# Performance work log

Measured on AMD Instinct MI355X. Metric: run time of the kernel, lower is better.

The kernel has to match this reference:

```python
import jax, jax.numpy as jnp
import numpy as np

B, CIN, H, W = 8, 4, 512, 512
HID, NCLS = 32, 19
WIN = 3
SCALE = 2


def conv(x, w, b, stride):
    # torch Conv2d(kernel=3, padding=1, stride=stride) equivalent
    y = jax.lax.conv_general_dilated(
        x, w, (stride, stride), [(1, 1), (1, 1)],
        dimension_numbers=('NCHW', 'OIHW', 'NCHW'))
    return y + b[None, :, None, None]


def interp_matrix(n_in, n_out, dtype):
    # 1D bilinear interpolation matrix, align_corners=True semantics
    pos = jnp.arange(n_out, dtype=dtype) * ((n_in - 1) / (n_out - 1))
    lo = jnp.clip(jnp.floor(pos).astype(jnp.int32), 0, n_in - 2)
    frac = pos - lo.astype(dtype)
    M = jnp.zeros((n_out, n_in), dtype)
    M = M.at[jnp.arange(n_out), lo].add(1 - frac)
    M = M.at[jnp.arange(n_out), lo + 1].add(frac)
    return M


def setup_inputs() -> dict:
    key = jax.random.key(0)
    ks = jax.random.split(key, 3)
    x = jax.random.normal(ks[0], (B, CIN, H, W), jnp.float32)
    w1 = jax.random.normal(ks[1], (HID, CIN, 3, 3), jnp.float32) * 0.1
    b1 = jnp.zeros((HID,), jnp.float32)
    w2 = jax.random.normal(ks[2], (NCLS, HID, 3, 3), jnp.float32) * 0.1
    b2 = jnp.zeros((NCLS,), jnp.float32)
    return {"x": x, "w1": w1, "b1": b1, "w2": w2, "b2": b2}


def reference(x, w1, b1, w2, b2):
    # --- cnn backbone -> class response maps ---
    h = jax.nn.relu(conv(x, w1, b1, 2))          # [B, HID, H/2, W/2]
    cmaps = conv(h, w2, b2, 1)                   # [B, NCLS, H/2, W/2]

    # --- bilinear upsample, align_corners=True (scale_factor=2) ---
    hi, wi = cmaps.shape[2], cmaps.shape[3]
    Mh = interp_matrix(hi, hi * SCALE, cmaps.dtype)
    Mw = interp_matrix(wi, wi * SCALE, cmaps.dtype)
    cmaps = jnp.einsum('oh,bchw,pw->bcop', Mh, cmaps, Mw)  # [B, NCLS, H, W]

    # --- peak stimulation: 3x3 local-max with -inf padding ---
    neg_inf = jnp.asarray(-jnp.inf, cmaps.dtype)
    local_max = jax.lax.reduce_window(
        cmaps, neg_inf, jax.lax.max,
        (1, 1, WIN, WIN), (1, 1, 1, 1),
        [(0, 0), (0, 0), (1, 1), (1, 1)])

    # median filter: per-(batch, class) spatial median threshold
    med = jnp.median(cmaps.reshape(cmaps.shape[0], cmaps.shape[1], -1), axis=2)
    med = med[:, :, None, None]

    peak_map = (cmaps == local_max) & (cmaps >= med)       # bool peak mask
    pf = peak_map.astype(cmaps.dtype)

    # aggregation: mean of map values at peaks -> class logits [B, NCLS]
    logits = (cmaps * pf).sum(axis=(2, 3)) / pf.sum(axis=(2, 3))
    return cmaps, logits
```

## Files before the change

kernel.cpp:

```cpp
#include <hip/hip_runtime.h>

#define B_ 8
#define CIN_ 4
#define H_ 512
#define W_ 512
#define HID_ 32
#define NCLS_ 19
#define HO_ 256
#define WO_ 256
#define UP_ 512
#define NPLANE (B_*NCLS_)
#define PLANE_ELEMS (UP_*UP_)
#define KMED1 131071u


__device__ __forceinline__ unsigned f2key(float f) {
  unsigned u = __float_as_uint(f);
  return (u & 0x80000000u) ? ~u : (u | 0x80000000u);
}
__device__ __forceinline__ float key2f(unsigned k) {
  unsigned u = (k & 0x80000000u) ? (k & 0x7FFFFFFFu) : ~k;
  return __uint_as_float(u);
}
__device__ __forceinline__ float ninf() { return __uint_as_float(0xFF800000u); }

__device__ __forceinline__ float up_val(const float* __restrict__ p, int oy, int ox) {
  const float s = (float)(255.0 / 511.0);
  float posy = (float)oy * s;
  int ly = (int)posy; if (ly > 254) ly = 254;
  float fy = posy - (float)ly;
  float posx = (float)ox * s;
  int lx = (int)posx; if (lx > 254) lx = 254;
  float fx = posx - (float)lx;
  const float* q = p + ly * WO_ + lx;
  float a = q[0], b = q[1], c = q[WO_], d = q[WO_ + 1];
  float r0 = fmaf(fx, b - a, a);
  float r1 = fmaf(fx, d - c, c);
  return fmaf(fy, r1 - r0, r0);
}

__global__ __launch_bounds__(256, 4) void conv1_kernel(
    const float* __restrict__ x, const float* __restrict__ w1,
    const float* __restrict__ b1, float* __restrict__ h) {
  int t = threadIdx.x & 63;
  int r = threadIdx.x >> 6;
  int oh = blockIdx.x * 4 + r;
  int b  = blockIdx.z;
  int ow0 = blockIdx.y * 128 + t * 2;
  int ic0 = 2 * ow0;

  float2 acc[HID_];
  #pragma unroll
  for (int oc = 0; oc < HID_; ++oc) {
    float bb = b1[oc];
    acc[oc].x = bb; acc[oc].y = bb;
  }

  #pragma unroll
  for (int ci = 0; ci < CIN_; ++ci) {
    const float* xp = x + ((size_t)(b * CIN_ + ci)) * H_ * W_;
    float4 A0, A1, A2;
    float lm[3];
    #pragma unroll
    for (int kh = 0; kh < 3; ++kh) {
      int ih = 2 * oh + kh - 1;
      float4 Av; float lv = 0.f;
      if ((unsigned)ih < (unsigned)H_) {
        const float* row = xp + ih * W_;
        Av = *reinterpret_cast<const float4*>(row + ic0);
        lv = (ic0 > 0) ? row[ic0 - 1] : 0.f;
      } else {
        Av.x = 0.f; Av.y = 0.f; Av.z = 0.f; Av.w = 0.f;
      }
      if (kh == 0) A0 = Av; else if (kh == 1) A1 = Av; else A2 = Av;
      lm[kh] = lv;
    }
    #pragma unroll
    for (int oc = 0; oc < HID_; ++oc) {
      const float* wp = w1 + ((size_t)oc * CIN_ + ci) * 9;
      {
        float w0 = wp[0], w1v = wp[1], w2v = wp[2];
        acc[oc].x += w0 * lm[0] + w1v * A0.x + w2v * A0.y;
        acc[oc].y += w0 * A0.y  + w1v * A0.z + w2v * A0.w;
      }
      {
        float w0 = wp[3], w1v = wp[4], w2v = wp[5];
        acc[oc].x += w0 * lm[1] + w1v * A1.x + w2v * A1.y;
        acc[oc].y += w0 * A1.y  + w1v * A1.z + w2v * A1.w;
      }
      {
        float w0 = wp[6], w1v = wp[7], w2v = wp[8];
        acc[oc].x += w0 * lm[2] + w1v * A2.x + w2v * A2.y;
        acc[oc].y += w0 * A2.y  + w1v * A2.z + w2v * A2.w;
      }
    }
  }
  #pragma unroll
  for (int oc = 0; oc < HID_; ++oc) {
    float2 o;
    o.x = fmaxf(acc[oc].x, 0.f); o.y = fmaxf(acc[oc].y, 0.f);
    *reinterpret_cast<float2*>(h + (((size_t)(b * HID_ + oc) * HO_ + oh) * WO_ + ow0)) = o;
  }
}

__global__ __launch_bounds__(256, 4) void conv2_kernel(
    const float* __restrict__ h, const float* __restrict__ w2,
    const float* __restrict__ b2, float* __restrict__ c0) {
  int t = threadIdx.x & 63;
  int r = threadIdx.x >> 6;
  int oh = blockIdx.x * 4 + r;
  int b  = blockIdx.z;
  int ow0 = blockIdx.y * 128 + t * 2;

  float2 acc[NCLS_];
  #pragma unroll
  for (int oc = 0; oc < NCLS_; ++oc) {
    float bb = b2[oc];
    acc[oc].x = bb; acc[oc].y = bb;
  }

  for (int ci = 0; ci < HID_; ++ci) {
    const float* hp = h + ((size_t)(b * HID_ + ci)) * HO_ * WO_;
    float2 M0, M1, M2;
    float L[3], R[3];
    #pragma unroll
    for (int kh = 0; kh < 3; ++kh) {
      int ih = oh + kh - 1;
      float2 Mv;
      float lv = 0.f, rv = 0.f;
      if ((unsigned)ih < (unsigned)HO_) {
        const float* row = hp + ih * WO_;
        Mv = *reinterpret_cast<const float2*>(row + ow0);
        lv = (ow0 > 0) ? row[ow0 - 1] : 0.f;
        rv = (ow0 + 2 < WO_) ? row[ow0 + 2] : 0.f;
      } else {
        Mv.x = 0.f; Mv.y = 0.f;
      }
      if (kh == 0) M0 = Mv; else if (kh == 1) M1 = Mv; else M2 = Mv;
      L[kh] = lv; R[kh] = rv;
    }
    const float* wpc = w2 + ci * 9;
    #pragma unroll
    for (int oc = 0; oc < NCLS_; ++oc) {
      const float* wp = wpc + oc * (HID_ * 9);
      {
        float w0 = wp[0], w1v = wp[1], w2v = wp[2];
        acc[oc].x += w0 * L[0]  + w1v * M0.x + w2v * M0.y;
        acc[oc].y += w0 * M0.x + w1v * M0.y + w2v * R[0];
      }
      {
        float w0 = wp[3], w1v = wp[4], w2v = wp[5];
        acc[oc].x += w0 * L[1]  + w1v * M1.x + w2v * M1.y;
        acc[oc].y += w0 * M1.x + w1v * M1.y + w2v * R[1];
      }
      {
        float w0 = wp[6], w1v = wp[7], w2v = wp[8];
        acc[oc].x += w0 * L[2]  + w1v * M2.x + w2v * M2.y;
        acc[oc].y += w0 * M2.x + w1v * M2.y + w2v * R[2];
      }
    }
  }
  #pragma unroll
  for (int oc = 0; oc < NCLS_; ++oc) {
    *reinterpret_cast<float2*>(c0 + (((size_t)(b * NCLS_ + oc) * HO_ + oh) * WO_ + ow0)) = acc[oc];
  }
}

__global__ __launch_bounds__(256) void upsample_kernel(
    const float* __restrict__ c0, float* __restrict__ out) {
  int tid = threadIdx.x;
  int oy = blockIdx.x * 2 + (tid >> 7);
  int t = tid & 127;
  int plane = blockIdx.y;
  const float* p = c0 + (size_t)plane * HO_ * WO_;
  int ox0 = t * 4;
  float4 o;
  o.x = up_val(p, oy, ox0 + 0);
  o.y = up_val(p, oy, ox0 + 1);
  o.z = up_val(p, oy, ox0 + 2);
  o.w = up_val(p, oy, ox0 + 3);
  *reinterpret_cast<float4*>(out + ((size_t)plane * UP_ + oy) * UP_ + ox0) = o;
}


__global__ void init_kernel(unsigned* kArr, unsigned* pvalArr, unsigned* gbArr,
                            unsigned* flagArr) {
  int i = threadIdx.x;
  if (i < NPLANE) { kArr[i] = KMED1; pvalArr[i] = 0u; gbArr[i] = 0u; flagArr[i] = 0u; }
}

__global__ __launch_bounds__(256) void hist_pass_kernel(
    const float* __restrict__ up, const unsigned* __restrict__ pvalArr,
    unsigned* __restrict__ ghist, int shift, unsigned bmask, unsigned fmask) {
  __shared__ unsigned lh[4 * 2048];
  int tid = threadIdx.x;
  int chunk = blockIdx.x;
  int plane = blockIdx.y;
  unsigned* mylh = lh + ((tid >> 6) << 11);
  for (int i = tid; i < 4 * 2048; i += 256) lh[i] = 0u;
  __syncthreads();
  unsigned fval = pvalArr[plane] & fmask;
  const float4* p4 = reinterpret_cast<const float4*>(up + (size_t)plane * PLANE_ELEMS)
                     + (size_t)chunk * 8192;
  #pragma unroll 4
  for (int it = 0; it < 32; ++it) {
    float4 v = p4[it * 256 + tid];
    unsigned k0 = f2key(v.x), k1 = f2key(v.y), k2 = f2key(v.z), k3 = f2key(v.w);
    if ((k0 & fmask) == fval) atomicAdd(&mylh[(k0 >> shift) & bmask], 1u);
    if ((k1 & fmask) == fval) atomicAdd(&mylh[(k1 >> shift) & bmask], 1u);
    if ((k2 & fmask) == fval) atomicAdd(&mylh[(k2 >> shift) & bmask], 1u);
    if ((k3 & fmask) == fval) atomicAdd(&mylh[(k3 >> shift) & bmask], 1u);
  }
  __syncthreads();
  for (int i = tid; i < 2048; i += 256) {
    unsigned c = lh[i] + lh[2048 + i] + lh[4096 + i] + lh[6144 + i];
    if (c) atomicAdd(&ghist[(size_t)plane * 2048 + i], c);
  }
}

__global__ __launch_bounds__(256) void select_kernel(
    unsigned* __restrict__ ghist, unsigned* kArr, unsigned* pvalArr, unsigned* gbArr,
    unsigned* v1Arr, unsigned* v2Arr, unsigned* flagArr,
    int shift, unsigned bmask, int nbins, int last) {
  __shared__ unsigned ssum[256], stmp[256];
  __shared__ unsigned sBin, sBelow, sCand[256];
  int tid = threadIdx.x;
  int plane = blockIdx.x;
  unsigned* hp = ghist + (size_t)plane * 2048;
  unsigned k = kArr[plane];
  unsigned lv[8];
  int b0 = tid * 8;
  unsigned lsum = 0;
  #pragma unroll
  for (int j = 0; j < 8; ++j) {
    unsigned c = (b0 + j < nbins) ? hp[b0 + j] : 0u;
    lv[j] = c; lsum += c;
  }
  ssum[tid] = lsum;
  __syncthreads();
  for (int off = 1; off < 256; off <<= 1) {
    stmp[tid] = (tid >= off) ? ssum[tid - off] : 0u; __syncthreads();
    ssum[tid] += stmp[tid]; __syncthreads();
  }
  unsigned incl = ssum[tid], excl = incl - lsum;
  if (excl <= k && k < incl) {
    unsigned kk = k - excl, below = excl;
    #pragma unroll
    for (int j = 0; j < 8; ++j) {
      if (kk < lv[j]) { sBin = (unsigned)(b0 + j); sBelow = below; break; }
      kk -= lv[j]; below += lv[j];
    }
  }
  __syncthreads();
  unsigned bin = sBin, below = sBelow;
  unsigned pvalNew = pvalArr[plane] | (bin << shift);
  unsigned gbNew = gbArr[plane] + below;
  if (!last) {
    for (int i = tid; i < 2048; i += 256) hp[i] = 0u;
    if (tid == 0) { kArr[plane] = k - below; pvalArr[plane] = pvalNew; gbArr[plane] = gbNew; }
  } else {
    unsigned cand = 0xFFFFFFFFu;
    #pragma unroll
    for (int j = 0; j < 8; ++j) {
      int g = b0 + j;
      if (g > (int)bin && g < nbins && lv[j] > 0u && (unsigned)g < cand) cand = (unsigned)g;
    }
    sCand[tid] = cand;
    __syncthreads();
    for (int s = 128; s > 0; s >>= 1) {
      if (tid < s) { unsigned o = sCand[tid + s]; if (o < sCand[tid]) sCand[tid] = o; }
      __syncthreads();
    }
    if (tid == 0) {
      unsigned ceq = hp[bin];
      v1Arr[plane] = pvalNew;
      if (131072u < gbNew + ceq) {
        v2Arr[plane] = pvalNew; flagArr[plane] = 0u;
      } else if (sCand[0] != 0xFFFFFFFFu) {
        v2Arr[plane] = (pvalNew & ~(bmask << shift)) | (sCand[0] << shift);
        flagArr[plane] = 0u;
      } else {
        v2Arr[plane] = 0xFFFFFFFFu; flagArr[plane] = 1u;
      }
    }
  }
}

__global__ __launch_bounds__(256) void minabove_kernel(
    const float* __restrict__ up, const unsigned* __restrict__ flagArr,
    const unsigned* __restrict__ v1Arr, unsigned* __restrict__ v2Arr) {
  int plane = blockIdx.y, chunk = blockIdx.x, tid = threadIdx.x;
  if (!flagArr[plane]) return;
  unsigned v1 = v1Arr[plane];
  const float4* base = reinterpret_cast<const float4*>(up + (size_t)plane * PLANE_ELEMS)
                       + (size_t)chunk * 4096;
  unsigned m = 0xFFFFFFFFu;
  for (int it = 0; it < 16; ++it) {
    float4 v = base[it * 256 + tid];
    unsigned k;
    k = f2key(v.x); if (k > v1 && k < m) m = k;
    k = f2key(v.y); if (k > v1 && k < m) m = k;
    k = f2key(v.z); if (k > v1 && k < m) m = k;
    k = f2key(v.w); if (k > v1 && k < m) m = k;
  }
  for (int off = 32; off > 0; off >>= 1) {
    unsigned o = __shfl_down(m, off, 64);
    if (o < m) m = o;
  }
  if ((tid & 63) == 0) atomicMin(&v2Arr[plane], m);
}

__global__ void finalize_kernel(const unsigned* __restrict__ v1Arr,
                                const unsigned* __restrict__ v2Arr,
                                float* __restrict__ med) {
  int i = threadIdx.x;
  if (i < NPLANE) med[i] = 0.5f * (key2f(v1Arr[i]) + key2f(v2Arr[i]));
}

__device__ __forceinline__ void row_load(const float* __restrict__ p, int y, int x0,
                                         float4& v, float& l, float& r) {
  if ((unsigned)y >= (unsigned)UP_) {
    float ni = ninf();
    v.x = v.y = v.z = v.w = ni; l = ni; r = ni;
    return;
  }
  const float* row = p + y * UP_ + x0;
  v = *reinterpret_cast<const float4*>(row);
  l = (x0 > 0) ? row[-1] : ninf();
  r = (x0 < UP_ - 4) ? row[4] : ninf();
}
__device__ __forceinline__ float4 hmax4(const float4& v, float l, float r) {
  float4 h;
  h.x = fmaxf(fmaxf(l, v.x), v.y);
  h.y = fmaxf(fmaxf(v.x, v.y), v.z);
  h.z = fmaxf(fmaxf(v.y, v.z), v.w);
  h.w = fmaxf(fmaxf(v.z, v.w), r);
  return h;
}

__global__ __launch_bounds__(256) void peak2_kernel(
    const float* __restrict__ cm, const float* __restrict__ med_arr,
    float* __restrict__ sums, float* __restrict__ cnts) {
  int tid = threadIdx.x;
  int plane = blockIdx.x;
  int strip = tid & 127;
  int ychunk = blockIdx.y * 2 + (tid >> 7);
  int x0 = strip * 4;
  int ystart = ychunk * 64;
  const float* p = cm + (size_t)plane * PLANE_ELEMS;
  float med = med_arr[plane];

  float4 v, vn; float l, r;
  row_load(p, ystart - 1, x0, v, l, r);
  float4 hprev = hmax4(v, l, r);
  row_load(p, ystart, x0, v, l, r);
  float4 hcur = hmax4(v, l, r);
  float4 vcur = v;

  float lsum = 0.f; int lcnt = 0;
  for (int yi = 0; yi < 64; ++yi) {
    int y = ystart + yi;
    float ln, rn;
    row_load(p, y + 1, x0, vn, ln, rn);
    float4 hnext = hmax4(vn, ln, rn);
    float mx = fmaxf(fmaxf(hprev.x, hcur.x), hnext.x);
    float my = fmaxf(fmaxf(hprev.y, hcur.y), hnext.y);
    float mz = fmaxf(fmaxf(hprev.z, hcur.z), hnext.z);
    float mw = fmaxf(fmaxf(hprev.w, hcur.w), hnext.w);
    if (vcur.x == mx && vcur.x >= med) { lsum += vcur.x; ++lcnt; }
    if (vcur.y == my && vcur.y >= med) { lsum += vcur.y; ++lcnt; }
    if (vcur.z == mz && vcur.z >= med) { lsum += vcur.z; ++lcnt; }
    if (vcur.w == mw && vcur.w >= med) { lsum += vcur.w; ++lcnt; }
    hprev = hcur; hcur = hnext; vcur = vn;
  }

  __shared__ float ss[256];
  __shared__ int sc[256];
  ss[tid] = lsum; sc[tid] = lcnt;
  __syncthreads();
  for (int s = 128; s > 0; s >>= 1) {
    if (tid < s) { ss[tid] += ss[tid + s]; sc[tid] += sc[tid + s]; }
    __syncthreads();
  }
  if (tid == 0) {
    atomicAdd(&sums[plane], ss[0]);
    atomicAdd(&cnts[plane], (float)sc[0]);
  }
}

__global__ void logits_kernel(const float* __restrict__ sums,
                              const float* __restrict__ cnts,
                              float* __restrict__ out) {
  int i = threadIdx.x;
  if (i < NPLANE) out[i] = sums[i] / cnts[i];
}

extern "C" void kernel_launch(void* const* d_in, const int* in_sizes, int n_in,
                              void* d_out, int out_size, void* d_ws, size_t ws_size,
                              hipStream_t stream) {
  const float* x  = (const float*)d_in[0];
  const float* w1 = (const float*)d_in[1];
  const float* b1 = (const float*)d_in[2];
  const float* w2 = (const float*)d_in[3];
  const float* b2 = (const float*)d_in[4];
  float* out = (float*)d_out;

  float* ws = (float*)d_ws;
  float* c0 = ws;
  unsigned* hist    = (unsigned*)(ws + 9961472);
  unsigned* kArr    = hist + 311296;
  unsigned* pvalArr = kArr + NPLANE;
  unsigned* gbArr   = pvalArr + NPLANE;
  unsigned* v1Arr   = gbArr + NPLANE;
  unsigned* v2Arr   = v1Arr + NPLANE;
  unsigned* flagArr = v2Arr + NPLANE;
  float* med  = (float*)(flagArr + NPLANE);
  float* sums = med + NPLANE;
  float* cnts = sums + NPLANE;
  float* h = out;

  init_kernel<<<1, 256, 0, stream>>>(kArr, pvalArr, gbArr, flagArr);
  hipMemsetAsync(hist, 0, (size_t)NPLANE * 2048 * sizeof(unsigned), stream);
  hipMemsetAsync(sums, 0, 2 * NPLANE * sizeof(float), stream);

  conv1_kernel<<<dim3(64, 2, 8), 256, 0, stream>>>(x, w1, b1, h);
  conv2_kernel<<<dim3(64, 2, 8), 256, 0, stream>>>(h, w2, b2, c0);
  upsample_kernel<<<dim3(256, NPLANE), 256, 0, stream>>>(c0, out);

  hist_pass_kernel<<<dim3(8, NPLANE), 256, 0, stream>>>(out, pvalArr, hist, 21, 0x7FFu, 0x00000000u);
  select_kernel<<<dim3(NPLANE), 256, 0, stream>>>(hist, kArr, pvalArr, gbArr,
      v1Arr, v2Arr, flagArr, 21, 0x7FFu, 2048, 0);
  hist_pass_kernel<<<dim3(8, NPLANE), 256, 0, stream>>>(out, pvalArr, hist, 10, 0x7FFu, 0xFFE00000u);
  select_kernel<<<dim3(NPLANE), 256, 0, stream>>>(hist, kArr, pvalArr, gbArr,
      v1Arr, v2Arr, flagArr, 10, 0x7FFu, 2048, 0);
  hist_pass_kernel<<<dim3(8, NPLANE), 256, 0, stream>>>(out, pvalArr, hist, 0, 0x3FFu, 0xFFFFFC00u);
  select_kernel<<<dim3(NPLANE), 256, 0, stream>>>(hist, kArr, pvalArr, gbArr,
      v1Arr, v2Arr, flagArr, 0, 0x3FFu, 1024, 1);
  minabove_kernel<<<dim3(16, NPLANE), 256, 0, stream>>>(out, flagArr, v1Arr, v2Arr);
  finalize_kernel<<<1, 256, 0, stream>>>(v1Arr, v2Arr, med);

  peak2_kernel<<<dim3(NPLANE, 4), 256, 0, stream>>>(out, med, sums, cnts);
  logits_kernel<<<1, 192, 0, stream>>>(sums, cnts, out + (out_size - NPLANE));
}
```

Measured before the change: 532.6 us.

## Split conv output channels across blocks and fuse first histogram into upsample

Both conv kernels now split their output channels into two groups handled by separate blocks. This halves accumulator registers per thread and doubles the grid, and launch bounds are raised to 8 blocks per CU to improve occupancy, at the cost of reloading the input rows once per group. The upsample kernel now also builds the first-pass radix histogram in shared memory as it writes each value, which removes a separate full read of the upsampled output. The fused kernel uses fewer, larger blocks and adds LDS atomics to the upsample path.

```diff
diff --git a/kernel.cpp b/kernel.cpp
--- a/kernel.cpp
+++ b/kernel.cpp
@@ -39,23 +39,18 @@
   return fmaf(fy, r1 - r0, r0);
 }
 
-__global__ __launch_bounds__(256, 4) void conv1_kernel(
+template<int OC0, int OC1>
+__device__ __forceinline__ void conv1_core(
     const float* __restrict__ x, const float* __restrict__ w1,
-    const float* __restrict__ b1, float* __restrict__ h) {
-  int t = threadIdx.x & 63;
-  int r = threadIdx.x >> 6;
-  int oh = blockIdx.x * 4 + r;
-  int b  = blockIdx.z;
-  int ow0 = blockIdx.y * 128 + t * 2;
+    const float* __restrict__ b1, float* __restrict__ h,
+    int oh, int b, int ow0) {
   int ic0 = 2 * ow0;
-
-  float2 acc[HID_];
-  #pragma unroll
-  for (int oc = 0; oc < HID_; ++oc) {
-    float bb = b1[oc];
-    acc[oc].x = bb; acc[oc].y = bb;
-  }
-
+  float2 acc[OC1 - OC0];
+  #pragma unroll
+  for (int j = 0; j < OC1 - OC0; ++j) {
+    float bb = b1[OC0 + j];
+    acc[j].x = bb; acc[j].y = bb;
+  }
   #pragma unroll
   for (int ci = 0; ci < CIN_; ++ci) {
     const float* xp = x + ((size_t)(b * CIN_ + ci)) * H_ * W_;
@@ -76,49 +71,58 @@
       lm[kh] = lv;
     }
     #pragma unroll
-    for (int oc = 0; oc < HID_; ++oc) {
-      const float* wp = w1 + ((size_t)oc * CIN_ + ci) * 9;
+    for (int j = 0; j < OC1 - OC0; ++j) {
+      const float* wp = w1 + ((size_t)(OC0 + j) * CIN_ + ci) * 9;
       {
         float w0 = wp[0], w1v = wp[1], w2v = wp[2];
-        acc[oc].x += w0 * lm[0] + w1v * A0.x + w2v * A0.y;
-        acc[oc].y += w0 * A0.y  + w1v * A0.z + w2v * A0.w;
+        acc[j].x += w0 * lm[0] + w1v * A0.x + w2v * A0.y;
+        acc[j].y += w0 * A0.y  + w1v * A0.z + w2v * A0.w;
       }
       {
         float w0 = wp[3], w1v = wp[4], w2v = wp[5];
-        acc[oc].x += w0 * lm[1] + w1v * A1.x + w2v * A1.y;
-        acc[oc].y += w0 * A1.y  + w1v * A1.z + w2v * A1.w;
+        acc[j].x += w0 * lm[1] + w1v * A1.x + w2v * A1.y;
+        acc[j].y += w0 * A1.y  + w1v * A1.z + w2v * A1.w;
       }
       {
         float w0 = wp[6], w1v = wp[7], w2v = wp[8];
-        acc[oc].x += w0 * lm[2] + w1v * A2.x + w2v * A2.y;
-        acc[oc].y += w0 * A2.y  + w1v * A2.z + w2v * A2.w;
-      }
-    }
-  }
-  #pragma unroll
-  for (int oc = 0; oc < HID_; ++oc) {
+        acc[j].x += w0 * lm[2] + w1v * A2.x + w2v * A2.y;
+        acc[j].y += w0 * A2.y  + w1v * A2.z + w2v * A2.w;
+      }
+    }
+  }
+  #pragma unroll
+  for (int j = 0; j < OC1 - OC0; ++j) {
     float2 o;
-    o.x = fmaxf(acc[oc].x, 0.f); o.y = fmaxf(acc[oc].y, 0.f);
-    *reinterpret_cast<float2*>(h + (((size_t)(b * HID_ + oc) * HO_ + oh) * WO_ + ow0)) = o;
-  }
-}
-
-__global__ __launch_bounds__(256, 4) void conv2_kernel(
-    const float* __restrict__ h, const float* __restrict__ w2,
-    const float* __restrict__ b2, float* __restrict__ c0) {
+    o.x = fmaxf(acc[j].x, 0.f); o.y = fmaxf(acc[j].y, 0.f);
+    *reinterpret_cast<float2*>(h + (((size_t)(b * HID_ + OC0 + j) * HO_ + oh) * WO_ + ow0)) = o;
+  }
+}
+
+__global__ __launch_bounds__(256, 8) void conv1_kernel(
+    const float* __restrict__ x, const float* __restrict__ w1,
+    const float* __restrict__ b1, float* __restrict__ h) {
   int t = threadIdx.x & 63;
   int r = threadIdx.x >> 6;
   int oh = blockIdx.x * 4 + r;
   int b  = blockIdx.z;
-  int ow0 = blockIdx.y * 128 + t * 2;
-
-  float2 acc[NCLS_];
-  #pragma unroll
-  for (int oc = 0; oc < NCLS_; ++oc) {
-    float bb = b2[oc];
-    acc[oc].x = bb; acc[oc].y = bb;
-  }
-
+  int colh = blockIdx.y & 1;
+  int ocg  = blockIdx.y >> 1;
+  int ow0 = colh * 128 + t * 2;
+  if (ocg == 0) conv1_core<0, 16>(x, w1, b1, h, oh, b, ow0);
+  else          conv1_core<16, 32>(x, w1, b1, h, oh, b, ow0);
+}
+
+template<int OC0, int OC1>
+__device__ __forceinline__ void conv2_core(
+    const float* __restrict__ h, const float* __restrict__ w2,
+    const float* __restrict__ b2, float* __restrict__ c0,
+    int oh, int b, int ow0) {
+  float2 acc[OC1 - OC0];
+  #pragma unroll
+  for (int j = 0; j < OC1 - OC0; ++j) {
+    float bb = b2[OC0 + j];
+    acc[j].x = bb; acc[j].y = bb;
+  }
   for (int ci = 0; ci < HID_; ++ci) {
     const float* hp = h + ((size_t)(b * HID_ + ci)) * HO_ * WO_;
     float2 M0, M1, M2;
@@ -141,45 +145,77 @@
     }
     const float* wpc = w2 + ci * 9;
     #pragma unroll
-    for (int oc = 0; oc < NCLS_; ++oc) {
-      const float* wp = wpc + oc * (HID_ * 9);
+    for (int j = 0; j < OC1 - OC0; ++j) {
+      const float* wp = wpc + (size_t)(OC0 + j) * (HID_ * 9);
       {
         float w0 = wp[0], w1v = wp[1], w2v = wp[2];
-        acc[oc].x += w0 * L[0]  + w1v * M0.x + w2v * M0.y;
-        acc[oc].y += w0 * M0.x + w1v * M0.y + w2v * R[0];
+        acc[j].x += w0 * L[0]  + w1v * M0.x + w2v * M0.y;
+        acc[j].y += w0 * M0.x + w1v * M0.y + w2v * R[0];
       }
       {
         float w0 = wp[3], w1v = wp[4], w2v = wp[5];
-        acc[oc].x += w0 * L[1]  + w1v * M1.x + w2v * M1.y;
-        acc[oc].y += w0 * M1.x + w1v * M1.y + w2v * R[1];
+        acc[j].x += w0 * L[1]  + w1v * M1.x + w2v * M1.y;
+        acc[j].y += w0 * M1.x + w1v * M1.y + w2v * R[1];
       }
       {
         float w0 = wp[6], w1v = wp[7], w2v = wp[8];
-        acc[oc].x += w0 * L[2]  + w1v * M2.x + w2v * M2.y;
-        acc[oc].y += w0 * M2.x + w1v * M2.y + w2v * R[2];
-      }
-    }
-  }
-  #pragma unroll
-  for (int oc = 0; oc < NCLS_; ++oc) {
-    *reinterpret_cast<float2*>(c0 + (((size_t)(b * NCLS_ + oc) * HO_ + oh) * WO_ + ow0)) = acc[oc];
-  }
-}
-
-__global__ __launch_bounds__(256) void upsample_kernel(
-    const float* __restrict__ c0, float* __restrict__ out) {
+        acc[j].x += w0 * L[2]  + w1v * M2.x + w2v * M2.y;
+        acc[j].y += w0 * M2.x + w1v * M2.y + w2v * R[2];
+      }
+    }
+  }
+  #pragma unroll
+  for (int j = 0; j < OC1 - OC0; ++j) {
+    *reinterpret_cast<float2*>(c0 + (((size_t)(b * NCLS_ + OC0 + j) * HO_ + oh) * WO_ + ow0)) = acc[j];
+  }
+}
+
+__global__ __launch_bounds__(256, 8) void conv2_kernel(
+    const float* __restrict__ h, const float* __restrict__ w2,
+    const float* __restrict__ b2, float* __restrict__ c0) {
+  int t = threadIdx.x & 63;
+  int r = threadIdx.x >> 6;
+  int oh = blockIdx.x * 4 + r;
+  int b  = blockIdx.z;
+  int colh = blockIdx.y & 1;
+  int ocg  = blockIdx.y >> 1;
+  int ow0 = colh * 128 + t * 2;
+  if (ocg == 0) conv2_core<0, 10>(h, w2, b2, c0, oh, b, ow0);
+  else          conv2_core<10, 19>(h, w2, b2, c0, oh, b, ow0);
+}
+
+__global__ __launch_bounds__(256) void upsample_hist_kernel(
+    const float* __restrict__ c0, float* __restrict__ out,
+    unsigned* __restrict__ ghist) {
+  __shared__ unsigned lh[4 * 2048];
   int tid = threadIdx.x;
-  int oy = blockIdx.x * 2 + (tid >> 7);
-  int t = tid & 127;
+  int chunk = blockIdx.x;
   int plane = blockIdx.y;
+  unsigned* mylh = lh + ((tid >> 6) << 11);
+  for (int i = tid; i < 4 * 2048; i += 256) lh[i] = 0u;
+  __syncthreads();
   const float* p = c0 + (size_t)plane * HO_ * WO_;
-  int ox0 = t * 4;
-  float4 o;
-  o.x = up_val(p, oy, ox0 + 0);
-  o.y = up_val(p, oy, ox0 + 1);
-  o.z = up_val(p, oy, ox0 + 2);
-  o.w = up_val(p, oy, ox0 + 3);
-  *reinterpret_cast<float4*>(out + ((size_t)plane * UP_ + oy) * UP_ + ox0) = o;
+  float* op = out + (size_t)plane * PLANE_ELEMS;
+  int ox0 = (tid & 127) * 4;
+  #pragma unroll 2
+  for (int it = 0; it < 32; ++it) {
+    int oy = chunk * 64 + it * 2 + (tid >> 7);
+    float4 o;
+    o.x = up_val(p, oy, ox0 + 0);
+    o.y = up_val(p, oy, ox0 + 1);
+    o.z = up_val(p, oy, ox0 + 2);
+    o.w = up_val(p, oy, ox0 + 3);
+    *reinterpret_cast<float4*>(op + (size_t)oy * UP_ + ox0) = o;
+    atomicAdd(&mylh[f2key(o.x) >> 21], 1u);
+    atomicAdd(&mylh[f2key(o.y) >> 21], 1u);
+    atomicAdd(&mylh[f2key(o.z) >> 21], 1u);
+    atomicAdd(&mylh[f2key(o.w) >> 21], 1u);
+  }
+  __syncthreads();
+  for (int i = tid; i < 2048; i += 256) {
+    unsigned c = lh[i] + lh[2048 + i] + lh[4096 + i] + lh[6144 + i];
+    if (c) atomicAdd(&ghist[(size_t)plane * 2048 + i], c);
+  }
 }
 
 
@@ -423,11 +459,10 @@
   hipMemsetAsync(hist, 0, (size_t)NPLANE * 2048 * sizeof(unsigned), stream);
   hipMemsetAsync(sums, 0, 2 * NPLANE * sizeof(float), stream);
 
-  conv1_kernel<<<dim3(64, 2, 8), 256, 0, stream>>>(x, w1, b1, h);
-  conv2_kernel<<<dim3(64, 2, 8), 256, 0, stream>>>(h, w2, b2, c0);
-  upsample_kernel<<<dim3(256, NPLANE), 256, 0, stream>>>(c0, out);
-
-  hist_pass_kernel<<<dim3(8, NPLANE), 256, 0, stream>>>(out, pvalArr, hist, 21, 0x7FFu, 0x00000000u);
+  conv1_kernel<<<dim3(64, 4, 8), 256, 0, stream>>>(x, w1, b1, h);
+  conv2_kernel<<<dim3(64, 4, 8), 256, 0, stream>>>(h, w2, b2, c0);
+
+  upsample_hist_kernel<<<dim3(8, NPLANE), 256, 0, stream>>>(c0, out, hist);
   select_kernel<<<dim3(NPLANE), 256, 0, stream>>>(hist, kArr, pvalArr, gbArr,
       v1Arr, v2Arr, flagArr, 21, 0x7FFu, 2048, 0);
   hist_pass_kernel<<<dim3(8, NPLANE), 256, 0, stream>>>(out, pvalArr, hist, 10, 0x7FFu, 0xFFE00000u);
```

New measurement: 559.9 us. +5.1%, slower.
